# Kernel tuning notes

Measured on AMD Instinct MI355X. Metric: run time of the kernel, lower is better.

## Reference

```python
import jax, jax.numpy as jnp
import numpy as np

B, S, T, I, H = 256, 128, 64, 63, 1024


def setup_inputs() -> dict:
    key = jax.random.key(0)
    ks = jax.random.split(key, 12)
    sc = 1.0 / np.sqrt(H)

    def rn(k, shape, scale=1.0):
        return jax.random.normal(k, shape, dtype=jnp.float32) * scale

    return dict(
        encoder_inputs=rn(ks[0], (B, S, I)),
        decoder_inputs=rn(ks[1], (B, T, I)),
        # encoder GRU params (PyTorch layout: [3H, in], gate order r,z,n)
        enc_Wih=rn(ks[2], (3 * H, I), sc), enc_Whh=rn(ks[3], (3 * H, H), sc),
        enc_bih=rn(ks[4], (3 * H,), sc), enc_bhh=rn(ks[5], (3 * H,), sc),
        # decoder GRUCell params (input dim = I, see notes)
        dec_Wih=rn(ks[6], (3 * H, I), sc), dec_Whh=rn(ks[7], (3 * H, H), sc),
        dec_bih=rn(ks[8], (3 * H,), sc), dec_bhh=rn(ks[9], (3 * H,), sc),
        # projector Linear(H -> I)
        proj_W=rn(ks[10], (I, H), sc), proj_b=rn(ks[11], (I,), sc),
    )


def _gru_gates(gi, gh, h):
    # gi = W_ih x + b_ih, gh = W_hh h + b_hh; PyTorch gate order (r, z, n)
    i_r, i_z, i_n = jnp.split(gi, 3, axis=-1)
    h_r, h_z, h_n = jnp.split(gh, 3, axis=-1)
    r = jax.nn.sigmoid(i_r + h_r)
    z = jax.nn.sigmoid(i_z + h_z)
    n = jnp.tanh(i_n + r * h_n)
    return (1.0 - z) * n + z * h


def reference(encoder_inputs, decoder_inputs, enc_Wih, enc_Whh, enc_bih,
              enc_bhh, dec_Wih, dec_Whh, dec_bih, dec_bhh, proj_W, proj_b):
    hid = enc_Whh.shape[1]
    b = encoder_inputs.shape[0]
    # ---- encoder GRU (batch_first), input-side gates precomputed as one GEMM
    gi_all = jnp.einsum('bsi,gi->bsg', encoder_inputs, enc_Wih) + enc_bih  # (B,S,3H)

    def step(h, gi):
        gh = h @ enc_Whh.T + enc_bhh
        return _gru_gates(gi, gh, h), None

    h0 = jnp.zeros((b, hid), encoder_inputs.dtype)
    enc_h, _ = jax.lax.scan(step, h0, jnp.swapaxes(gi_all, 0, 1))  # (B,H) final hidden

    # ---- decoder: per the source, every timestep feeds the SAME encoder
    # hidden state into the GRUCell (state is not carried), so all timesteps
    # are independent and can be computed as batched GEMMs over (B,T).
    gi_dec = jnp.einsum('bti,gi->btg', decoder_inputs, dec_Wih) + dec_bih   # (B,T,3H)
    gh_dec = (enc_h @ dec_Whh.T + dec_bhh)[:, None, :]                       # (B,1,3H)
    next_states = _gru_gates(gi_dec, gh_dec, enc_h[:, None, :])              # (B,T,H)

    # dropout p=0.0 (identity); projector Linear
    outputs = jnp.einsum('bth,oh->bto', next_states, proj_W) + proj_b       # (B,T,I)
    return outputs
```

## Files before the change

kernel.cpp:

```cpp
#include <hip/hip_runtime.h>


typedef unsigned short u16;
typedef unsigned int   u32;
typedef __attribute__((ext_vector_type(8))) short s8v;
typedef __attribute__((ext_vector_type(4))) float f4v;
typedef __attribute__((ext_vector_type(4))) int  i4v;
typedef __attribute__((ext_vector_type(4))) unsigned int u4v;

__device__ __forceinline__ float b2f(u16 u) {
    return __uint_as_float(((u32)u) << 16);
}
__device__ __forceinline__ u16 f2b(float f) {
    u32 x = __float_as_uint(f);
    u32 r = x + 0x7fffu + ((x >> 16) & 1u);
    return (u16)(r >> 16);
}
__device__ __forceinline__ float sigf(float x) {
    return 1.0f / (1.0f + __expf(-x));
}
__device__ __forceinline__ f4v mfma16(s8v a, s8v b, f4v c) {
    return __builtin_amdgcn_mfma_f32_16x16x32_bf16(a, b, c, 0, 0, 0);
}
__device__ __forceinline__ void unpack8(u4v w0, u4v w1, s8v& hi, s8v& lo) {
    u32 c0 = w0[0], c1 = w0[1], c2 = w0[2], c3 = w0[3];
    u32 c4 = w1[0], c5 = w1[1], c6 = w1[2], c7 = w1[3];
    union { u32 u[4]; s8v v; } H, L;
    H.u[0] = (c0 & 0xffffu) | (c1 << 16);
    H.u[1] = (c2 & 0xffffu) | (c3 << 16);
    H.u[2] = (c4 & 0xffffu) | (c5 << 16);
    H.u[3] = (c6 & 0xffffu) | (c7 << 16);
    L.u[0] = (c0 >> 16) | (c1 & 0xffff0000u);
    L.u[1] = (c2 >> 16) | (c3 & 0xffff0000u);
    L.u[2] = (c4 >> 16) | (c5 & 0xffff0000u);
    L.u[3] = (c6 >> 16) | (c7 & 0xffff0000u);
    hi = H.v; lo = L.v;
}

__global__ void zero_ws(i4v* __restrict__ p, int n) {
    int i = blockIdx.x * blockDim.x + threadIdx.x;
    if (i < n) { i4v z = {0, 0, 0, 0}; p[i] = z; }
}

__global__ void conv_wih_split_pad(const float* __restrict__ s,
                                   u16* __restrict__ hi, u16* __restrict__ lo) {
    int idx = blockIdx.x * blockDim.x + threadIdx.x;
    int row = idx >> 6, col = idx & 63;
    float v = (col < 63) ? s[(size_t)row * 63 + col] : 0.f;
    u16 h = f2b(v);
    hi[idx] = h;
    lo[idx] = f2b(v - b2f(h));
}

__global__ void conv_pw_split_pad(const float* __restrict__ s,
                                  u16* __restrict__ hi, u16* __restrict__ lo) {
    int idx = blockIdx.x * blockDim.x + threadIdx.x;
    float v = (idx < 63 * 1024) ? s[idx] : 0.f;
    u16 h = f2b(v);
    hi[idx] = h;
    lo[idx] = f2b(v - b2f(h));
}

__global__ __launch_bounds__(512, 1) void enc_persist8(
    const float* __restrict__ Whh,
    const u16* __restrict__ WihH, const u16* __restrict__ WihL,
    const float* __restrict__ bih, const float* __restrict__ bhh,
    const float* __restrict__ xenc,
    u32* __restrict__ hbuf,
    int* __restrict__ ep)
{
    __shared__ f4v red[8][4][3][64];
    __shared__ u16 WisH[48 * 72];
    __shared__ u16 WisL[48 * 72];

    __builtin_amdgcn_fence(__ATOMIC_ACQUIRE, "agent");

    const int tid  = threadIdx.x;
    const int lane = tid & 63;
    const int wave = tid >> 6;
    const int lrow = lane & 15;
    const int lk8  = lane >> 4;
    const int bid = blockIdx.x;
    const int xcd = bid & 7;
    const int y   = bid >> 3;
    const int mt  = y & 3;
    const int jt  = xcd * 8 + (y >> 2);
    const int m0 = mt * 64;
    const int j0 = jt * 16;

    int* subCtr  = ep + (mt * 8 + xcd) * 16;
    int* waveCtr = ep + (mt * 8 + wave) * 16;

    if (tid < 192) {
        int wr = tid >> 2, qq = tid & 3;
        int grow = (wr >> 4) * 1024 + j0 + (wr & 15);
        const u16* wpH = WihH + (size_t)grow * 64 + qq * 16;
        const u16* wpL = WihL + (size_t)grow * 64 + qq * 16;
        *(i4v*)&WisH[wr * 72 + qq * 16]     = *(const i4v*)wpH;
        *(i4v*)&WisH[wr * 72 + qq * 16 + 8] = *(const i4v*)(wpH + 8);
        *(i4v*)&WisL[wr * 72 + qq * 16]     = *(const i4v*)wpL;
        *(i4v*)&WisL[wr * 72 + qq * 16 + 8] = *(const i4v*)(wpL + 8);
    }

    s8v bHf[3][4], bLf[3][4];
    const int k0 = wave * 128;
    #pragma unroll
    for (int gg = 0; gg < 3; ++gg)
        #pragma unroll
        for (int ks = 0; ks < 4; ++ks) {
            const float* p = Whh + (size_t)(gg * 1024 + j0 + lrow) * 1024 +
                             k0 + ks * 32 + lk8 * 8;
            f4v a = *(const f4v*)p;
            f4v b = *(const f4v*)(p + 4);
            union { u16 a[8]; s8v v; } H, L;
            #pragma unroll
            for (int j = 0; j < 8; ++j) {
                float v = (j < 4) ? a[j] : b[j - 4];
                u16 hh = f2b(v);
                H.a[j] = hh;
                L.a[j] = f2b(v - b2f(hh));
            }
            bHf[gg][ks] = H.v;
            bLf[gg][ks] = L.v;
        }

    const int jcol = j0 + lrow;
    const float bhr = bhh[jcol], bhz = bhh[1024 + jcol], bhn = bhh[2048 + jcol];
    const float bir = bih[jcol], biz = bih[1024 + jcol], bin = bih[2048 + jcol];

    size_t aoff[4];
    #pragma unroll
    for (int mtile = 0; mtile < 4; ++mtile)
        aoff[mtile] = (size_t)(m0 + mtile * 16 + lrow) * 1024 + k0 + lk8 * 8;

    const float* xrow = xenc + (size_t)(m0 + (wave & 3) * 16 + lrow) * 8064;
    float hprev[4] = {0.f, 0.f, 0.f, 0.f};

    float xf[16];
    if (wave < 4) {
        #pragma unroll
        for (int ks = 0; ks < 2; ++ks)
            #pragma unroll
            for (int j = 0; j < 8; ++j) {
                int col = ks * 32 + lk8 * 8 + j;
                xf[ks * 8 + j] = (col < 63) ? xrow[col] : 0.f;
            }
    }

    __syncthreads();

    for (int s = 0; s < 128; ++s) {
        const u32* hin = hbuf + (size_t)s * 262144;
        u32* hout      = hbuf + (size_t)(s + 1) * 262144;

        f4v gi_r = {0.f, 0.f, 0.f, 0.f};
        f4v gi_z = {0.f, 0.f, 0.f, 0.f};
        f4v gi_n = {0.f, 0.f, 0.f, 0.f};
        if (wave < 4) {
            #pragma unroll
            for (int ks = 0; ks < 2; ++ks) {
                union { u16 a[8]; s8v v; } xh, xl;
                #pragma unroll
                for (int j = 0; j < 8; ++j) {
                    float v = xf[ks * 8 + j];
                    u16 hh = f2b(v);
                    xh.a[j] = hh;
                    xl.a[j] = f2b(v - b2f(hh));
                }
                int ao = ks * 32 + lk8 * 8;
                s8v brh = *(const s8v*)&WisH[(lrow) * 72 + ao];
                s8v brl = *(const s8v*)&WisL[(lrow) * 72 + ao];
                s8v bzh = *(const s8v*)&WisH[(16 + lrow) * 72 + ao];
                s8v bzl = *(const s8v*)&WisL[(16 + lrow) * 72 + ao];
                s8v bnh = *(const s8v*)&WisH[(32 + lrow) * 72 + ao];
                s8v bnl = *(const s8v*)&WisL[(32 + lrow) * 72 + ao];
                gi_r = mfma16(xh.v, brh, gi_r);
                gi_r = mfma16(xh.v, brl, gi_r);
                gi_r = mfma16(xl.v, brh, gi_r);
                gi_z = mfma16(xh.v, bzh, gi_z);
                gi_z = mfma16(xh.v, bzl, gi_z);
                gi_z = mfma16(xl.v, bzh, gi_z);
                gi_n = mfma16(xh.v, bnh, gi_n);
                gi_n = mfma16(xh.v, bnl, gi_n);
                gi_n = mfma16(xl.v, bnh, gi_n);
            }
        }

        if (s) {
            const int tgt = s * 8;
            while (__hip_atomic_load(waveCtr, __ATOMIC_RELAXED,
                                     __HIP_MEMORY_SCOPE_SYSTEM) < tgt)
                __builtin_amdgcn_s_sleep(1);
        }

        f4v accr[4], accz[4], acchn[4];
        #pragma unroll
        for (int m = 0; m < 4; ++m) {
            accr[m]  = f4v{0.f, 0.f, 0.f, 0.f};
            accz[m]  = f4v{0.f, 0.f, 0.f, 0.f};
            acchn[m] = f4v{0.f, 0.f, 0.f, 0.f};
        }
        #pragma unroll
        for (int mtile = 0; mtile < 4; ++mtile) {
            #pragma unroll
            for (int ks = 0; ks < 4; ++ks) {
                const u32* p = hin + aoff[mtile] + ks * 32;
                u4v w0 = *(const u4v*)p;
                u4v w1 = *(const u4v*)(p + 4);
                s8v ahi, alo;
                unpack8(w0, w1, ahi, alo);
                accr[mtile]  = mfma16(ahi, bHf[0][ks], accr[mtile]);
                accr[mtile]  = mfma16(ahi, bLf[0][ks], accr[mtile]);
                accr[mtile]  = mfma16(alo, bHf[0][ks], accr[mtile]);
                accz[mtile]  = mfma16(ahi, bHf[1][ks], accz[mtile]);
                accz[mtile]  = mfma16(ahi, bLf[1][ks], accz[mtile]);
                accz[mtile]  = mfma16(alo, bHf[1][ks], accz[mtile]);
                acchn[mtile] = mfma16(ahi, bHf[2][ks], acchn[mtile]);
                acchn[mtile] = mfma16(ahi, bLf[2][ks], acchn[mtile]);
                acchn[mtile] = mfma16(alo, bHf[2][ks], acchn[mtile]);
            }
        }

        #pragma unroll
        for (int m = 0; m < 4; ++m) {
            red[wave][m][0][lane] = accr[m];
            red[wave][m][1][lane] = accz[m];
            red[wave][m][2][lane] = acchn[m];
        }
        __syncthreads();

        if (wave < 4) {
            f4v sr = {0.f, 0.f, 0.f, 0.f};
            f4v sz = {0.f, 0.f, 0.f, 0.f};
            f4v sh = {0.f, 0.f, 0.f, 0.f};
            #pragma unroll
            for (int w = 0; w < 8; ++w) {
                sr += red[w][wave][0][lane];
                sz += red[w][wave][1][lane];
                sh += red[w][wave][2][lane];
            }
            #pragma unroll
            for (int reg = 0; reg < 4; ++reg) {
                int brow = m0 + wave * 16 + lk8 * 4 + reg;
                float rr = sigf(sr[reg] + gi_r[reg] + bir + bhr);
                float zz = sigf(sz[reg] + gi_z[reg] + biz + bhz);
                float nn = tanhf(gi_n[reg] + bin + rr * (sh[reg] + bhn));
                float h = (1.f - zz) * nn + zz * hprev[reg];
                u16 hh = f2b(h);
                u16 ll = f2b(h - b2f(hh));
                hprev[reg] = b2f(hh) + b2f(ll);
                u32 pk = (u32)hh | ((u32)ll << 16);
                __hip_atomic_store(&hout[(size_t)brow * 1024 + jcol], pk,
                                   __ATOMIC_RELAXED, __HIP_MEMORY_SCOPE_SYSTEM);
            }
        }

        __syncthreads();
        if (tid == 0)
            __hip_atomic_fetch_add(subCtr, 1, __ATOMIC_RELAXED,
                                   __HIP_MEMORY_SCOPE_SYSTEM);
        if (wave < 4) {
            int sn = (s < 127) ? s + 1 : 127;
            const float* xr = xrow + sn * 63;
            #pragma unroll
            for (int ks = 0; ks < 2; ++ks)
                #pragma unroll
                for (int j = 0; j < 8; ++j) {
                    int col = ks * 32 + lk8 * 8 + j;
                    xf[ks * 8 + j] = (col < 63) ? xr[col] : 0.f;
                }
        }
    }
}

__global__ __launch_bounds__(256, 1) void gru_gemm1(
    const float* __restrict__ Whh,
    const float* __restrict__ bhh,
    const u32* __restrict__ hin,
    float* __restrict__ gh_out)
{
    __shared__ u16 WbH[48 * 264];
    __shared__ u16 WbL[48 * 264];

    const int tid  = threadIdx.x;
    const int lane = tid & 63;
    const int wave = tid >> 6;
    const int lrow = lane & 15;
    const int lk8  = lane >> 4;
    const int mt = blockIdx.x & 3;
    const int jt = blockIdx.x >> 2;
    const int m0 = mt * 64;
    const int j0 = jt * 16;

    f4v acc_r  = {0.f, 0.f, 0.f, 0.f};
    f4v acc_z  = {0.f, 0.f, 0.f, 0.f};
    f4v acc_hn = {0.f, 0.f, 0.f, 0.f};

    f4v stgA[6], stgB[6];
    #pragma unroll
    for (int i = 0; i < 6; ++i) {
        int c16 = i * 256 + tid;
        int row = c16 >> 5, p16 = c16 & 31;
        int grow = (row >> 4) * 1024 + j0 + (row & 15);
        const float* p = Whh + (size_t)grow * 1024 + p16 * 8;
        stgA[i] = *(const f4v*)p;
        stgB[i] = *(const f4v*)(p + 4);
    }
    #pragma unroll
    for (int i = 0; i < 6; ++i) {
        int c16 = i * 256 + tid;
        int row = c16 >> 5, p16 = c16 & 31;
        union { u16 a[8]; i4v v; } H, L;
        #pragma unroll
        for (int j = 0; j < 8; ++j) {
            float v = (j < 4) ? stgA[i][j] : stgB[i][j - 4];
            u16 hh = f2b(v);
            H.a[j] = hh;
            L.a[j] = f2b(v - b2f(hh));
        }
        *(i4v*)&WbH[row * 264 + p16 * 8] = H.v;
        *(i4v*)&WbL[row * 264 + p16 * 8] = L.v;
    }
    __syncthreads();

    const size_t arow = (size_t)(m0 + wave * 16 + lrow) * 1024 + lk8 * 8;
    const u32* hp = hin + arow;

    for (int c = 0; c < 4; ++c) {
        if (c < 3) {
            #pragma unroll
            for (int i = 0; i < 6; ++i) {
                int c16 = i * 256 + tid;
                int row = c16 >> 5, p16 = c16 & 31;
                int grow = (row >> 4) * 1024 + j0 + (row & 15);
                const float* p = Whh + (size_t)grow * 1024 + (c + 1) * 256 + p16 * 8;
                stgA[i] = *(const f4v*)p;
                stgB[i] = *(const f4v*)(p + 4);
            }
        }
        #pragma unroll
        for (int ks = 0; ks < 8; ++ks) {
            int kk = c * 256 + ks * 32;
            int bo = ks * 32 + lk8 * 8;
            u4v w0 = *(const u4v*)(hp + kk);
            u4v w1 = *(const u4v*)(hp + kk + 4);
            s8v ahi, alo;
            unpack8(w0, w1, ahi, alo);
            s8v brh = *(const s8v*)&WbH[(lrow) * 264 + bo];
            s8v brl = *(const s8v*)&WbL[(lrow) * 264 + bo];
            s8v bzh = *(const s8v*)&WbH[(16 + lrow) * 264 + bo];
            s8v bzl = *(const s8v*)&WbL[(16 + lrow) * 264 + bo];
            s8v bnh = *(const s8v*)&WbH[(32 + lrow) * 264 + bo];
            s8v bnl = *(const s8v*)&WbL[(32 + lrow) * 264 + bo];
            acc_r  = mfma16(ahi, brh, acc_r);
            acc_r  = mfma16(ahi, brl, acc_r);
            acc_r  = mfma16(alo, brh, acc_r);
            acc_z  = mfma16(ahi, bzh, acc_z);
            acc_z  = mfma16(ahi, bzl, acc_z);
            acc_z  = mfma16(alo, bzh, acc_z);
            acc_hn = mfma16(ahi, bnh, acc_hn);
            acc_hn = mfma16(ahi, bnl, acc_hn);
            acc_hn = mfma16(alo, bnh, acc_hn);
        }
        __syncthreads();
        if (c < 3) {
            #pragma unroll
            for (int i = 0; i < 6; ++i) {
                int c16 = i * 256 + tid;
                int row = c16 >> 5, p16 = c16 & 31;
                union { u16 a[8]; i4v v; } H, L;
                #pragma unroll
                for (int j = 0; j < 8; ++j) {
                    float v = (j < 4) ? stgA[i][j] : stgB[i][j - 4];
                    u16 hh = f2b(v);
                    H.a[j] = hh;
                    L.a[j] = f2b(v - b2f(hh));
                }
                *(i4v*)&WbH[row * 264 + p16 * 8] = H.v;
                *(i4v*)&WbL[row * 264 + p16 * 8] = L.v;
            }
            __syncthreads();
        }
    }

    const int jcol = j0 + lrow;
    const float bhr = bhh[jcol];
    const float bhz = bhh[1024 + jcol];
    const float bhn = bhh[2048 + jcol];
    #pragma unroll
    for (int reg = 0; reg < 4; ++reg) {
        int brow = m0 + wave * 16 + lk8 * 4 + reg;
        gh_out[(size_t)brow * 3072 + jcol]        = acc_r[reg] + bhr;
        gh_out[(size_t)brow * 3072 + 1024 + jcol] = acc_z[reg] + bhz;
        gh_out[(size_t)brow * 3072 + 2048 + jcol] = acc_hn[reg] + bhn;
    }
}

__global__ __launch_bounds__(256, 1) void dec_fused(
    const u16* __restrict__ WihH, const u16* __restrict__ WihL,
    const float* __restrict__ bih,
    const float* __restrict__ xdec,
    const u32* __restrict__ e32,
    const float* __restrict__ gh,
    const u16* __restrict__ pWH, const u16* __restrict__ pWL,
    const float* __restrict__ pb,
    float* __restrict__ out)
{
    __shared__ u16 XdH[64 * 72];
    __shared__ u16 XdL[64 * 72];
    __shared__ u16 WiH_[192 * 72];
    __shared__ u16 WiL_[192 * 72];
    __shared__ u16 nsH[64 * 72];
    __shared__ u16 nsL[64 * 72];

    const int tid  = threadIdx.x;
    const int lane = tid & 63;
    const int wave = tid >> 6;
    const int lrow = lane & 15;
    const int lk8  = lane >> 4;
    const int b    = blockIdx.x;

    {
        int row = tid >> 2, q = tid & 3;
        const float* xr = xdec + (size_t)(b * 64 + row) * 63;
        #pragma unroll
        for (int ii = 0; ii < 16; ++ii) {
            int col = q * 16 + ii;
            float v = (col < 63) ? xr[col] : 0.f;
            u16 hh = f2b(v);
            XdH[row * 72 + col] = hh;
            XdL[row * 72 + col] = f2b(v - b2f(hh));
        }
    }

    f4v oacc[4];
    #pragma unroll
    for (int f = 0; f < 4; ++f) oacc[f] = f4v{0.f, 0.f, 0.f, 0.f};

    for (int j0 = 0; j0 < 1024; j0 += 64) {
        #pragma unroll
        for (int k = 0; k < 3; ++k) {
            int c = tid + k * 256;
            int r = c >> 2, qq = c & 3;
            int grow = (r >> 6) * 1024 + j0 + (r & 63);
            const u16* srcH = WihH + (size_t)grow * 64 + qq * 16;
            const u16* srcL = WihL + (size_t)grow * 64 + qq * 16;
            *(i4v*)&WiH_[r * 72 + qq * 16]     = *(const i4v*)srcH;
            *(i4v*)&WiH_[r * 72 + qq * 16 + 8] = *(const i4v*)(srcH + 8);
            *(i4v*)&WiL_[r * 72 + qq * 16]     = *(const i4v*)srcL;
            *(i4v*)&WiL_[r * 72 + qq * 16 + 8] = *(const i4v*)(srcL + 8);
        }
        __syncthreads();

        f4v ar[4], az[4], an[4];
        #pragma unroll
        for (int jf = 0; jf < 4; ++jf) {
            ar[jf] = f4v{0.f, 0.f, 0.f, 0.f};
            az[jf] = f4v{0.f, 0.f, 0.f, 0.f};
            an[jf] = f4v{0.f, 0.f, 0.f, 0.f};
        }
        #pragma unroll
        for (int ks = 0; ks < 2; ++ks) {
            int ao = ks * 32 + lk8 * 8;
            s8v ah = *(const s8v*)&XdH[(wave * 16 + lrow) * 72 + ao];
            s8v al = *(const s8v*)&XdL[(wave * 16 + lrow) * 72 + ao];
            #pragma unroll
            for (int jf = 0; jf < 4; ++jf) {
                s8v brh = *(const s8v*)&WiH_[(jf * 16 + lrow) * 72 + ao];
                s8v brl = *(const s8v*)&WiL_[(jf * 16 + lrow) * 72 + ao];
                s8v bzh = *(const s8v*)&WiH_[(64 + jf * 16 + lrow) * 72 + ao];
                s8v bzl = *(const s8v*)&WiL_[(64 + jf * 16 + lrow) * 72 + ao];
                s8v bnh = *(const s8v*)&WiH_[(128 + jf * 16 + lrow) * 72 + ao];
                s8v bnl = *(const s8v*)&WiL_[(128 + jf * 16 + lrow) * 72 + ao];
                ar[jf] = mfma16(ah, brh, ar[jf]);
                ar[jf] = mfma16(ah, brl, ar[jf]);
                ar[jf] = mfma16(al, brh, ar[jf]);
                az[jf] = mfma16(ah, bzh, az[jf]);
                az[jf] = mfma16(ah, bzl, az[jf]);
                az[jf] = mfma16(al, bzh, az[jf]);
                an[jf] = mfma16(ah, bnh, an[jf]);
                an[jf] = mfma16(ah, bnl, an[jf]);
                an[jf] = mfma16(al, bnh, an[jf]);
            }
        }

        #pragma unroll
        for (int jf = 0; jf < 4; ++jf) {
            int j = j0 + jf * 16 + lrow;
            float ghr = gh[(size_t)b * 3072 + j];
            float ghz = gh[(size_t)b * 3072 + 1024 + j];
            float ghn = gh[(size_t)b * 3072 + 2048 + j];
            float bir = bih[j];
            float biz = bih[1024 + j];
            float bin = bih[2048 + j];
            u32 pk = e32[(size_t)b * 1024 + j];
            float he = b2f((u16)(pk & 0xffffu)) + b2f((u16)(pk >> 16));
            #pragma unroll
            for (int reg = 0; reg < 4; ++reg) {
                float r  = sigf(ar[jf][reg] + bir + ghr);
                float z  = sigf(az[jf][reg] + biz + ghz);
                float nn = tanhf(an[jf][reg] + bin + r * ghn);
                float v  = (1.f - z) * nn + z * he;
                u16 hh = f2b(v);
                int lo_i = (wave * 16 + lk8 * 4 + reg) * 72 + jf * 16 + lrow;
                nsH[lo_i] = hh;
                nsL[lo_i] = f2b(v - b2f(hh));
            }
        }
        __syncthreads();

        #pragma unroll
        for (int ks = 0; ks < 2; ++ks) {
            int ao = ks * 32 + lk8 * 8;
            s8v ah = *(const s8v*)&nsH[(wave * 16 + lrow) * 72 + ao];
            s8v al = *(const s8v*)&nsL[(wave * 16 + lrow) * 72 + ao];
            #pragma unroll
            for (int f = 0; f < 4; ++f) {
                size_t bo = (size_t)(f * 16 + lrow) * 1024 + j0 + ks * 32 + lk8 * 8;
                s8v bh = *(const s8v*)(pWH + bo);
                s8v bl = *(const s8v*)(pWL + bo);
                oacc[f] = mfma16(ah, bh, oacc[f]);
                oacc[f] = mfma16(ah, bl, oacc[f]);
                oacc[f] = mfma16(al, bh, oacc[f]);
            }
        }
        __syncthreads();
    }

    #pragma unroll
    for (int f = 0; f < 4; ++f) {
        int o = f * 16 + lrow;
        if (o < 63) {
            float pbv = pb[o];
            #pragma unroll
            for (int reg = 0; reg < 4; ++reg) {
                int t = wave * 16 + lk8 * 4 + reg;
                out[((size_t)(b * 64 + t)) * 63 + o] = oacc[f][reg] + pbv;
            }
        }
    }
}

extern "C" void kernel_launch(void* const* d_in, const int* in_sizes, int n_in,
                              void* d_out, int out_size, void* d_ws, size_t ws_size,
                              hipStream_t stream)
{
    const float* enc_x = (const float*)d_in[0];
    const float* dec_x = (const float*)d_in[1];
    const float* eWih  = (const float*)d_in[2];
    const float* eWhh  = (const float*)d_in[3];
    const float* ebih  = (const float*)d_in[4];
    const float* ebhh  = (const float*)d_in[5];
    const float* dWih  = (const float*)d_in[6];
    const float* dWhh  = (const float*)d_in[7];
    const float* dbih  = (const float*)d_in[8];
    const float* dbhh  = (const float*)d_in[9];
    const float* pW    = (const float*)d_in[10];
    const float* pb    = (const float*)d_in[11];

    char* ws = (char*)d_ws;

    u32*   hbuf  = (u32*)(ws);
    int*   ep    = (int*)(ws + 135266304);
    float* ghd   = (float*)(ws + 135282688);
    u16*   eWihH = (u16*)(ws + 138428416);
    u16*   eWihL = (u16*)(ws + 138821632);
    u16*   dWihH = (u16*)(ws + 139214848);
    u16*   dWihL = (u16*)(ws + 139608064);
    u16*   pWH   = (u16*)(ws + 140001280);
    u16*   pWL   = (u16*)(ws + 140132352);

    conv_wih_split_pad<<<dim3(768), dim3(256), 0, stream>>>(eWih, eWihH, eWihL);
    conv_wih_split_pad<<<dim3(768), dim3(256), 0, stream>>>(dWih, dWihH, dWihL);
    conv_pw_split_pad<<<dim3(256), dim3(256), 0, stream>>>(pW, pWH, pWL);

    zero_ws<<<dim3(256), dim3(256), 0, stream>>>((i4v*)hbuf, 65536);
    zero_ws<<<dim3(4), dim3(256), 0, stream>>>((i4v*)ep, 1024);

    enc_persist8<<<dim3(256), dim3(512), 0, stream>>>(
        eWhh, eWihH, eWihL, ebih, ebhh, enc_x, hbuf, ep);

    u32* Hfin = hbuf + (size_t)128 * 262144;

    gru_gemm1<<<dim3(256), dim3(256), 0, stream>>>(dWhh, dbhh, Hfin, ghd);

    dec_fused<<<dim3(256), dim3(256), 0, stream>>>(
        dWihH, dWihL, dbih, dec_x, Hfin, ghd, pWH, pWL, pb, (float*)d_out);
}
```

Measured before the change: 1.520 ms.

## Merge prologue kernels, use per-wave arrival counters, interleave MFMA chains

The five setup kernels (weight hi/lo split conversions and workspace zeroing) become one prologue launch, cutting launch overhead. In the encoder's per-step barrier, each of the four writer waves now waits for its own hidden-state stores and then increments the arrival counter itself. The target count rises from 8 to 32 arrivals per step, so consumers no longer wait on a block-wide syncthreads before the signal. MFMA calls across the r/z/n gates are interleaved so independent accumulator chains can overlap and hide MFMA latency, at the cost of four times more atomic traffic on the counter.

```diff
diff --git a/kernel.cpp b/kernel.cpp
--- a/kernel.cpp
+++ b/kernel.cpp
@@ -37,31 +37,42 @@
     hi = H.v; lo = L.v;
 }
 
-__global__ void zero_ws(i4v* __restrict__ p, int n) {
-    int i = blockIdx.x * blockDim.x + threadIdx.x;
-    if (i < n) { i4v z = {0, 0, 0, 0}; p[i] = z; }
-}
-
-__global__ void conv_wih_split_pad(const float* __restrict__ s,
-                                   u16* __restrict__ hi, u16* __restrict__ lo) {
-    int idx = blockIdx.x * blockDim.x + threadIdx.x;
-    int row = idx >> 6, col = idx & 63;
-    float v = (col < 63) ? s[(size_t)row * 63 + col] : 0.f;
-    u16 h = f2b(v);
-    hi[idx] = h;
-    lo[idx] = f2b(v - b2f(h));
-}
-
-__global__ void conv_pw_split_pad(const float* __restrict__ s,
-                                  u16* __restrict__ hi, u16* __restrict__ lo) {
-    int idx = blockIdx.x * blockDim.x + threadIdx.x;
-    float v = (idx < 63 * 1024) ? s[idx] : 0.f;
-    u16 h = f2b(v);
-    hi[idx] = h;
-    lo[idx] = f2b(v - b2f(h));
-}
-
-__global__ __launch_bounds__(512, 1) void enc_persist8(
+__global__ __launch_bounds__(256) void prologue(
+    const float* __restrict__ eWih, const float* __restrict__ dWih,
+    const float* __restrict__ pW,
+    u16* __restrict__ eWihH, u16* __restrict__ eWihL,
+    u16* __restrict__ dWihH, u16* __restrict__ dWihL,
+    u16* __restrict__ pWH, u16* __restrict__ pWL,
+    i4v* __restrict__ hbuf0, i4v* __restrict__ ep)
+{
+    const int b = blockIdx.x;
+    const int tid = threadIdx.x;
+    if (b < 1536) {
+        const float* src = (b < 768) ? eWih : dWih;
+        u16* hi = (b < 768) ? eWihH : dWihH;
+        u16* lo = (b < 768) ? eWihL : dWihL;
+        int idx = ((b < 768) ? b : b - 768) * 256 + tid;
+        int row = idx >> 6, col = idx & 63;
+        float v = (col < 63) ? src[(size_t)row * 63 + col] : 0.f;
+        u16 h = f2b(v);
+        hi[idx] = h;
+        lo[idx] = f2b(v - b2f(h));
+    } else if (b < 1792) {
+        int idx = (b - 1536) * 256 + tid;
+        float v = (idx < 63 * 1024) ? pW[idx] : 0.f;
+        u16 h = f2b(v);
+        pWH[idx] = h;
+        pWL[idx] = f2b(v - b2f(h));
+    } else if (b < 2048) {
+        i4v z = {0, 0, 0, 0};
+        hbuf0[(b - 1792) * 256 + tid] = z;
+    } else {
+        i4v z = {0, 0, 0, 0};
+        for (int i = tid; i < 1024; i += 256) ep[i] = z;
+    }
+}
+
+__global__ __launch_bounds__(512, 1) void enc_persist13(
     const float* __restrict__ Whh,
     const u16* __restrict__ WihH, const u16* __restrict__ WihL,
     const float* __restrict__ bih, const float* __restrict__ bhh,
@@ -175,19 +186,19 @@
                 s8v bnh = *(const s8v*)&WisH[(32 + lrow) * 72 + ao];
                 s8v bnl = *(const s8v*)&WisL[(32 + lrow) * 72 + ao];
                 gi_r = mfma16(xh.v, brh, gi_r);
+                gi_z = mfma16(xh.v, bzh, gi_z);
+                gi_n = mfma16(xh.v, bnh, gi_n);
                 gi_r = mfma16(xh.v, brl, gi_r);
+                gi_z = mfma16(xh.v, bzl, gi_z);
+                gi_n = mfma16(xh.v, bnl, gi_n);
                 gi_r = mfma16(xl.v, brh, gi_r);
-                gi_z = mfma16(xh.v, bzh, gi_z);
-                gi_z = mfma16(xh.v, bzl, gi_z);
                 gi_z = mfma16(xl.v, bzh, gi_z);
-                gi_n = mfma16(xh.v, bnh, gi_n);
-                gi_n = mfma16(xh.v, bnl, gi_n);
                 gi_n = mfma16(xl.v, bnh, gi_n);
             }
         }
 
         if (s) {
-            const int tgt = s * 8;
+            const int tgt = s * 32;
             while (__hip_atomic_load(waveCtr, __ATOMIC_RELAXED,
                                      __HIP_MEMORY_SCOPE_SYSTEM) < tgt)
                 __builtin_amdgcn_s_sleep(1);
@@ -210,13 +221,13 @@
                 s8v ahi, alo;
                 unpack8(w0, w1, ahi, alo);
                 accr[mtile]  = mfma16(ahi, bHf[0][ks], accr[mtile]);
+                accz[mtile]  = mfma16(ahi, bHf[1][ks], accz[mtile]);
+                acchn[mtile] = mfma16(ahi, bHf[2][ks], acchn[mtile]);
                 accr[mtile]  = mfma16(ahi, bLf[0][ks], accr[mtile]);
+                accz[mtile]  = mfma16(ahi, bLf[1][ks], accz[mtile]);
+                acchn[mtile] = mfma16(ahi, bLf[2][ks], acchn[mtile]);
                 accr[mtile]  = mfma16(alo, bHf[0][ks], accr[mtile]);
-                accz[mtile]  = mfma16(ahi, bHf[1][ks], accz[mtile]);
-                accz[mtile]  = mfma16(ahi, bLf[1][ks], accz[mtile]);
                 accz[mtile]  = mfma16(alo, bHf[1][ks], accz[mtile]);
-                acchn[mtile] = mfma16(ahi, bHf[2][ks], acchn[mtile]);
-                acchn[mtile] = mfma16(ahi, bLf[2][ks], acchn[mtile]);
                 acchn[mtile] = mfma16(alo, bHf[2][ks], acchn[mtile]);
             }
         }
@@ -253,12 +264,13 @@
                 __hip_atomic_store(&hout[(size_t)brow * 1024 + jcol], pk,
                                    __ATOMIC_RELAXED, __HIP_MEMORY_SCOPE_SYSTEM);
             }
+            asm volatile("s_waitcnt vmcnt(0)" ::: "memory");
+            if (lane == 0)
+                __hip_atomic_fetch_add(subCtr, 1, __ATOMIC_RELAXED,
+                                       __HIP_MEMORY_SCOPE_SYSTEM);
         }
 
         __syncthreads();
-        if (tid == 0)
-            __hip_atomic_fetch_add(subCtr, 1, __ATOMIC_RELAXED,
-                                   __HIP_MEMORY_SCOPE_SYSTEM);
         if (wave < 4) {
             int sn = (s < 127) ? s + 1 : 127;
             const float* xr = xrow + sn * 63;
@@ -353,13 +365,13 @@
             s8v bnh = *(const s8v*)&WbH[(32 + lrow) * 264 + bo];
             s8v bnl = *(const s8v*)&WbL[(32 + lrow) * 264 + bo];
             acc_r  = mfma16(ahi, brh, acc_r);
+            acc_z  = mfma16(ahi, bzh, acc_z);
+            acc_hn = mfma16(ahi, bnh, acc_hn);
             acc_r  = mfma16(ahi, brl, acc_r);
+            acc_z  = mfma16(ahi, bzl, acc_z);
+            acc_hn = mfma16(ahi, bnl, acc_hn);
             acc_r  = mfma16(alo, brh, acc_r);
-            acc_z  = mfma16(ahi, bzh, acc_z);
-            acc_z  = mfma16(ahi, bzl, acc_z);
             acc_z  = mfma16(alo, bzh, acc_z);
-            acc_hn = mfma16(ahi, bnh, acc_hn);
-            acc_hn = mfma16(ahi, bnl, acc_hn);
             acc_hn = mfma16(alo, bnh, acc_hn);
         }
         __syncthreads();
@@ -473,13 +485,13 @@
                 s8v bnh = *(const s8v*)&WiH_[(128 + jf * 16 + lrow) * 72 + ao];
                 s8v bnl = *(const s8v*)&WiL_[(128 + jf * 16 + lrow) * 72 + ao];
                 ar[jf] = mfma16(ah, brh, ar[jf]);
+                az[jf] = mfma16(ah, bzh, az[jf]);
+                an[jf] = mfma16(ah, bnh, an[jf]);
                 ar[jf] = mfma16(ah, brl, ar[jf]);
+                az[jf] = mfma16(ah, bzl, az[jf]);
+                an[jf] = mfma16(ah, bnl, an[jf]);
                 ar[jf] = mfma16(al, brh, ar[jf]);
-                az[jf] = mfma16(ah, bzh, az[jf]);
-                az[jf] = mfma16(ah, bzl, az[jf]);
                 az[jf] = mfma16(al, bzh, az[jf]);
-                an[jf] = mfma16(ah, bnh, an[jf]);
-                an[jf] = mfma16(ah, bnl, an[jf]);
                 an[jf] = mfma16(al, bnh, an[jf]);
             }
         }
@@ -570,14 +582,11 @@
     u16*   pWH   = (u16*)(ws + 140001280);
     u16*   pWL   = (u16*)(ws + 140132352);
 
-    conv_wih_split_pad<<<dim3(768), dim3(256), 0, stream>>>(eWih, eWihH, eWihL);
-    conv_wih_split_pad<<<dim3(768), dim3(256), 0, stream>>>(dWih, dWihH, dWihL);
-    conv_pw_split_pad<<<dim3(256), dim3(256), 0, stream>>>(pW, pWH, pWL);
-
-    zero_ws<<<dim3(256), dim3(256), 0, stream>>>((i4v*)hbuf, 65536);
-    zero_ws<<<dim3(4), dim3(256), 0, stream>>>((i4v*)ep, 1024);
-
-    enc_persist8<<<dim3(256), dim3(512), 0, stream>>>(
+    prologue<<<dim3(2049), dim3(256), 0, stream>>>(
+        eWih, dWih, pW, eWihH, eWihL, dWihH, dWihL, pWH, pWL,
+        (i4v*)hbuf, (i4v*)ep);
+
+    enc_persist13<<<dim3(256), dim3(512), 0, stream>>>(
         eWhh, eWihH, eWihL, ebih, ebhh, enc_x, hbuf, ep);
 
     u32* Hfin = hbuf + (size_t)128 * 262144;
```

New measurement: 1.556 ms. 2.3% more time.
